# Kernel tuning notes

Measured on AMD Instinct MI355X. Metric: run time of the kernel, lower is better.

## Reference

```python
import jax, jax.numpy as jnp
import numpy as np

I, T, L, E, H, W = 256, 256, 32, 128, 7, 7

def setup_inputs() -> dict:
    key = jax.random.key(0)
    k1, k2, k3 = jax.random.split(key, 3)
    image_features = jax.random.normal(k1, (I, E, H, W), dtype=jnp.float32)
    text_features = jax.random.normal(k2, (T, L, E), dtype=jnp.float32)
    text_length = jax.random.randint(k3, (T,), 1, L + 1, dtype=jnp.int32)
    logit_neg_log_temperature = jnp.asarray(-np.log(0.07), dtype=jnp.float32)
    return {
        "image_features": image_features,
        "text_features": text_features,
        "text_length": text_length,
        "logit_neg_log_temperature": logit_neg_log_temperature,
    }

def reference(image_features, text_features, text_length, logit_neg_log_temperature):
    # image_features: [I, E, H, W]; text_features: [T, L, E]
    i, e, h, w = image_features.shape
    img = image_features.reshape(i, e, h * w)            # [I, E, HW]
    # cross-modal similarity per (image, text, token, patch): [I, T, L, HW]
    sim = jnp.einsum('iep,tle->itlp', img, text_features)
    # max over patches, then sum over tokens, normalized by caption length
    match_max = jnp.max(sim, axis=3)                     # [I, T, L]
    match = jnp.sum(match_max, axis=2) / text_length.astype(match_max.dtype)  # [I, T]
    logit_scale = jnp.exp(logit_neg_log_temperature)
    logits_per_image = match * logit_scale
    logits_per_text = match.T * logit_scale
    return (logits_per_image, logits_per_text)
```

## Files before the change

kernel.cpp:

```cpp
#include <hip/hip_runtime.h>
#include <hip/hip_bf16.h>

typedef __attribute__((ext_vector_type(8)))  short bf16x8;
typedef __attribute__((ext_vector_type(16))) float f32x16;

#define I_N 256
#define T_N 256
#define L_N 32
#define E_N 128
#define P_N 49
#define TG  4

__global__ __launch_bounds__(256) void pack_all(const float* __restrict__ txt,
                                                const float* __restrict__ img,
                                                unsigned short* __restrict__ bpre,
                                                unsigned short* __restrict__ apre) {
    const int bid = blockIdx.x;
    if (bid < 512) {
        int gid  = bid * 256 + threadIdx.x;
        int lane = gid & 63;
        int ks   = (gid >> 6) & 7;
        int t    = gid >> 9;
        int l    = lane & 31;
        int e0   = ks * 16 + (lane >> 5) * 8;
        const float* src = txt + (t * L_N + l) * E_N + e0;
        union { unsigned short u[8]; bf16x8 v; } o;
        #pragma unroll
        for (int j = 0; j < 8; ++j) {
            __hip_bfloat16 h = __float2bfloat16(src[j]);
            o.u[j] = *reinterpret_cast<unsigned short*>(&h);
        }
        ((bf16x8*)bpre)[gid] = o.v;
    } else {
        int gid   = (bid - 512) * 256 + threadIdx.x;
        int lane  = gid & 63;
        int ks    = (gid >> 6) & 7;
        int pt    = (gid >> 9) & 1;
        int i     = gid >> 10;
        int patch = pt * 32 + (lane & 31);
        int e0    = ks * 16 + (lane >> 5) * 8;
        const float* src = img + i * (E_N * P_N) + e0 * P_N + patch;
        union { unsigned short u[8]; bf16x8 v; } o;
        #pragma unroll
        for (int j = 0; j < 8; ++j) {
            float x = (patch < P_N) ? src[j * P_N] : 0.0f;
            __hip_bfloat16 h = __float2bfloat16(x);
            o.u[j] = *reinterpret_cast<unsigned short*>(&h);
        }
        ((bf16x8*)apre)[gid] = o.v;
    }
}

__global__ __launch_bounds__(256) void clip_mfma(
    const unsigned short* __restrict__ apre,
    const unsigned short* __restrict__ bpre,
    const int*   __restrict__ tlen,
    const float* __restrict__ nlt,
    float*       __restrict__ out) {

    __shared__ short sB[2][TG * 8 * 512];

    const int wid  = threadIdx.x >> 6;
    const int lane = threadIdx.x & 63;
    const int i    = blockIdx.y * 4 + wid;
    const int t0   = blockIdx.x * 16;
    const float scale = expf(nlt[0]);
    const bool  lo32  = (lane < 32);

    bf16x8 af[2][8];
    const bf16x8* ap = (const bf16x8*)apre + (size_t)i * 16 * 64;
    #pragma unroll
    for (int pt = 0; pt < 2; ++pt)
        #pragma unroll
        for (int ks = 0; ks < 8; ++ks)
            af[pt][ks] = ap[(pt * 8 + ks) * 64 + lane];

    auto stage = [&](int buf, int g) {
        #pragma unroll
        for (int q = 0; q < 8; ++q) {
            int fl = wid * 8 + q;
            int t  = t0 + g * TG + (fl >> 3);
            int f  = fl & 7;
            const unsigned short* src = bpre + ((size_t)(t * 8 + f)) * 512 + lane * 8;
            short* dst = &sB[buf][fl * 512];
            __builtin_amdgcn_global_load_lds(
                (const __attribute__((address_space(1))) unsigned int*)(const void*)src,
                (__attribute__((address_space(3))) unsigned int*)(void*)dst, 16, 0, 0);
        }
    };

    auto reduceT = [&](f32x16 (&a)[2], int t) {
        float m = a[0][0];
        #pragma unroll
        for (int r = 1; r < 16; ++r) m = fmaxf(m, a[0][r]);
        #pragma unroll
        for (int r = 0; r < 8; ++r)  m = fmaxf(m, a[1][r]);
        m = fmaxf(m, lo32 ? a[1][8] : -INFINITY);
        m = fmaxf(m, __shfl_xor(m, 32));
        float s = m;
        #pragma unroll
        for (int off = 1; off <= 16; off <<= 1)
            s += __shfl_xor(s, off);
        if (lane == 0) {
            float match = (s / (float)tlen[t]) * scale;
            out[i * T_N + t]             = match;
            out[I_N * T_N + t * I_N + i] = match;
        }
    };

    bf16x8 bf[2][8];
    f32x16 acc[2][2];

    stage(0, 0);
    __syncthreads();

    #pragma unroll
    for (int tx = 0; tx < 16; ++tx) {
        const int p   = tx & 1;
        const int gg  = tx >> 2;
        const int txg = tx & 3;

        if ((tx & 3) == 0) {
            if (tx > 0) __syncthreads();
            if (gg + 1 < 4) stage((gg + 1) & 1, gg + 1);
        }

        const bf16x8* bfp = (const bf16x8*)&sB[gg & 1][0];
        #pragma unroll
        for (int ks = 0; ks < 8; ++ks)
            bf[p][ks] = bfp[(txg * 8 + ks) * 64 + lane];

        #pragma unroll
        for (int pt = 0; pt < 2; ++pt)
            #pragma unroll
            for (int r = 0; r < 16; ++r)
                acc[p][pt][r] = 0.0f;

        #pragma unroll
        for (int ks = 0; ks < 8; ++ks)
            #pragma unroll
            for (int pt = 0; pt < 2; ++pt)
                acc[p][pt] = __builtin_amdgcn_mfma_f32_32x32x16_bf16(
                    af[pt][ks], bf[p][ks], acc[p][pt], 0, 0, 0);

        if (tx > 0) reduceT(acc[1 - p], t0 + tx - 1);
    }
    reduceT(acc[1], t0 + 15);
}

extern "C" void kernel_launch(void* const* d_in, const int* in_sizes, int n_in,
                              void* d_out, int out_size, void* d_ws, size_t ws_size,
                              hipStream_t stream) {
    const float* img  = (const float*)d_in[0];
    const float* txt  = (const float*)d_in[1];
    const int*   tlen = (const int*)d_in[2];
    const float* nlt  = (const float*)d_in[3];
    float*       out  = (float*)d_out;

    unsigned short* bpre = (unsigned short*)d_ws;
    unsigned short* apre = (unsigned short*)((char*)d_ws + (2u << 20));

    pack_all<<<1536, 256, 0, stream>>>(txt, img, bpre, apre);

    dim3 grid(16, 64);
    clip_mfma<<<grid, 256, 0, stream>>>(apre, bpre, tlen, nlt, out);
}
```

Before: 45.13 us.

## Software-pipeline LDS B-fragment loads ahead of MFMA and prefetch two stages

Restructures the t-loop so the B fragments for the next text are loaded from LDS while the current MFMA chain runs, using explicit ping-pong register sets instead of array indexing. It stages two text groups up front and issues the next global-to-LDS stage right after each barrier. MFMA sections are wrapped with s_setprio to favour matrix issue across waves. This aims to hide LDS read latency and staging latency behind compute, at the cost of extra register pressure from the doubled B fragments and more complex barrier placement.

```diff
diff --git a/kernel.cpp b/kernel.cpp
--- a/kernel.cpp
+++ b/kernel.cpp
@@ -89,6 +89,29 @@
         }
     };
 
+    auto loadB = [&](bf16x8 (&bf)[8], int buf, int txg) {
+        const bf16x8* bfp = (const bf16x8*)&sB[buf][0];
+        #pragma unroll
+        for (int ks = 0; ks < 8; ++ks)
+            bf[ks] = bfp[(txg * 8 + ks) * 64 + lane];
+    };
+
+    auto mfmaT = [&](f32x16 (&acc)[2], bf16x8 (&bf)[8]) {
+        #pragma unroll
+        for (int pt = 0; pt < 2; ++pt)
+            #pragma unroll
+            for (int r = 0; r < 16; ++r)
+                acc[pt][r] = 0.0f;
+        __builtin_amdgcn_s_setprio(1);
+        #pragma unroll
+        for (int ks = 0; ks < 8; ++ks)
+            #pragma unroll
+            for (int pt = 0; pt < 2; ++pt)
+                acc[pt] = __builtin_amdgcn_mfma_f32_32x32x16_bf16(
+                    af[pt][ks], bf[ks], acc[pt], 0, 0, 0);
+        __builtin_amdgcn_s_setprio(0);
+    };
+
     auto reduceT = [&](f32x16 (&a)[2], int t) {
         float m = a[0][0];
         #pragma unroll
@@ -108,44 +131,34 @@
         }
     };
 
-    bf16x8 bf[2][8];
-    f32x16 acc[2][2];
+    bf16x8 bfA[8], bfB[8];
+    f32x16 accA[2], accB[2];
 
     stage(0, 0);
+    stage(1, 1);
     __syncthreads();
+    loadB(bfA, 0, 0);
+
+    auto slot = [&](int tx, bf16x8 (&bfC)[8], f32x16 (&accC)[2],
+                    bf16x8 (&bfN)[8], f32x16 (&accP)[2]) {
+        const int g   = tx >> 2;
+        const int txg = tx & 3;
+        mfmaT(accC, bfC);
+        if (txg < 3) loadB(bfN, g & 1, txg + 1);
+        if (tx > 0)  reduceT(accP, t0 + tx - 1);
+        if (txg == 3 && tx + 1 < 16) {
+            __syncthreads();
+            if (g + 2 < 4) stage(g & 1, g + 2);
+            loadB(bfN, (g + 1) & 1, 0);
+        }
+    };
 
     #pragma unroll
-    for (int tx = 0; tx < 16; ++tx) {
-        const int p   = tx & 1;
-        const int gg  = tx >> 2;
-        const int txg = tx & 3;
-
-        if ((tx & 3) == 0) {
-            if (tx > 0) __syncthreads();
-            if (gg + 1 < 4) stage((gg + 1) & 1, gg + 1);
-        }
-
-        const bf16x8* bfp = (const bf16x8*)&sB[gg & 1][0];
-        #pragma unroll
-        for (int ks = 0; ks < 8; ++ks)
-            bf[p][ks] = bfp[(txg * 8 + ks) * 64 + lane];
-
-        #pragma unroll
-        for (int pt = 0; pt < 2; ++pt)
-            #pragma unroll
-            for (int r = 0; r < 16; ++r)
-                acc[p][pt][r] = 0.0f;
-
-        #pragma unroll
-        for (int ks = 0; ks < 8; ++ks)
-            #pragma unroll
-            for (int pt = 0; pt < 2; ++pt)
-                acc[p][pt] = __builtin_amdgcn_mfma_f32_32x32x16_bf16(
-                    af[pt][ks], bf[p][ks], acc[p][pt], 0, 0, 0);
-
-        if (tx > 0) reduceT(acc[1 - p], t0 + tx - 1);
+    for (int pr = 0; pr < 8; ++pr) {
+        slot(2 * pr,     bfA, accA, bfB, accB);
+        slot(2 * pr + 1, bfB, accB, bfA, accA);
     }
-    reduceT(acc[1], t0 + 15);
+    reduceT(accB, t0 + 15);
 }
 
 extern "C" void kernel_launch(void* const* d_in, const int* in_sizes, int n_in,
```

After: 47.03 us. 1.04x slower.

## Load text fragments directly from global, drop LDS staging and software pipelining

Applied to the files above, without the earlier changes.

Removes the double-buffered LDS staging via global_load_lds and the barriers between groups. Each wave now loads its B fragments straight from global memory (L2-cached) inside a non-unrolled loop. The kernel gets an occupancy hint of 3 blocks per CU and raises wave priority around the MFMA chain. This removes LDS traffic and block-wide syncs and should lower register pressure, but each wave re-reads B from global/L2 and loses the overlap between loads and the previous tile's reduction.

```diff
diff --git a/kernel.cpp b/kernel.cpp
--- a/kernel.cpp
+++ b/kernel.cpp
@@ -9,7 +9,6 @@
 #define L_N 32
 #define E_N 128
 #define P_N 49
-#define TG  4
 
 __global__ __launch_bounds__(256) void pack_all(const float* __restrict__ txt,
                                                 const float* __restrict__ img,
@@ -51,14 +50,12 @@
     }
 }
 
-__global__ __launch_bounds__(256) void clip_mfma(
+__global__ __launch_bounds__(256, 3) void clip_mfma(
     const unsigned short* __restrict__ apre,
     const unsigned short* __restrict__ bpre,
     const int*   __restrict__ tlen,
     const float* __restrict__ nlt,
     float*       __restrict__ out) {
-
-    __shared__ short sB[2][TG * 8 * 512];
 
     const int wid  = threadIdx.x >> 6;
     const int lane = threadIdx.x & 63;
@@ -75,77 +72,48 @@
         for (int ks = 0; ks < 8; ++ks)
             af[pt][ks] = ap[(pt * 8 + ks) * 64 + lane];
 
-    auto stage = [&](int buf, int g) {
+    const bf16x8* bp = (const bf16x8*)bpre;
+
+    #pragma unroll 1
+    for (int tx = 0; tx < 16; ++tx) {
+        const int t = t0 + tx;
+
+        bf16x8 bf[8];
+        const bf16x8* tb = bp + (size_t)t * 8 * 64;
         #pragma unroll
-        for (int q = 0; q < 8; ++q) {
-            int fl = wid * 8 + q;
-            int t  = t0 + g * TG + (fl >> 3);
-            int f  = fl & 7;
-            const unsigned short* src = bpre + ((size_t)(t * 8 + f)) * 512 + lane * 8;
-            short* dst = &sB[buf][fl * 512];
-            __builtin_amdgcn_global_load_lds(
-                (const __attribute__((address_space(1))) unsigned int*)(const void*)src,
-                (__attribute__((address_space(3))) unsigned int*)(void*)dst, 16, 0, 0);
+        for (int ks = 0; ks < 8; ++ks)
+            bf[ks] = tb[ks * 64 + lane];
+
+        f32x16 a0, a1;
+        #pragma unroll
+        for (int r = 0; r < 16; ++r) { a0[r] = 0.0f; a1[r] = 0.0f; }
+
+        __builtin_amdgcn_s_setprio(1);
+        #pragma unroll
+        for (int ks = 0; ks < 8; ++ks) {
+            a0 = __builtin_amdgcn_mfma_f32_32x32x16_bf16(af[0][ks], bf[ks], a0, 0, 0, 0);
+            a1 = __builtin_amdgcn_mfma_f32_32x32x16_bf16(af[1][ks], bf[ks], a1, 0, 0, 0);
         }
-    };
+        __builtin_amdgcn_s_setprio(0);
 
-    auto reduceT = [&](f32x16 (&a)[2], int t) {
-        float m = a[0][0];
+        float m = a0[0];
         #pragma unroll
-        for (int r = 1; r < 16; ++r) m = fmaxf(m, a[0][r]);
+        for (int r = 1; r < 16; ++r) m = fmaxf(m, a0[r]);
         #pragma unroll
-        for (int r = 0; r < 8; ++r)  m = fmaxf(m, a[1][r]);
-        m = fmaxf(m, lo32 ? a[1][8] : -INFINITY);
+        for (int r = 0; r < 8; ++r)  m = fmaxf(m, a1[r]);
+        m = fmaxf(m, lo32 ? a1[8] : -INFINITY);
         m = fmaxf(m, __shfl_xor(m, 32));
         float s = m;
         #pragma unroll
         for (int off = 1; off <= 16; off <<= 1)
             s += __shfl_xor(s, off);
+
         if (lane == 0) {
             float match = (s / (float)tlen[t]) * scale;
             out[i * T_N + t]             = match;
             out[I_N * T_N + t * I_N + i] = match;
         }
-    };
-
-    bf16x8 bf[2][8];
-    f32x16 acc[2][2];
-
-    stage(0, 0);
-    __syncthreads();
-
-    #pragma unroll
-    for (int tx = 0; tx < 16; ++tx) {
-        const int p   = tx & 1;
-        const int gg  = tx >> 2;
-        const int txg = tx & 3;
-
-        if ((tx & 3) == 0) {
-            if (tx > 0) __syncthreads();
-            if (gg + 1 < 4) stage((gg + 1) & 1, gg + 1);
-        }
-
-        const bf16x8* bfp = (const bf16x8*)&sB[gg & 1][0];
-        #pragma unroll
-        for (int ks = 0; ks < 8; ++ks)
-            bf[p][ks] = bfp[(txg * 8 + ks) * 64 + lane];
-
-        #pragma unroll
-        for (int pt = 0; pt < 2; ++pt)
-            #pragma unroll
-            for (int r = 0; r < 16; ++r)
-                acc[p][pt][r] = 0.0f;
-
-        #pragma unroll
-        for (int ks = 0; ks < 8; ++ks)
-            #pragma unroll
-            for (int pt = 0; pt < 2; ++pt)
-                acc[p][pt] = __builtin_amdgcn_mfma_f32_32x32x16_bf16(
-                    af[pt][ks], bf[p][ks], acc[p][pt], 0, 0, 0);
-
-        if (tx > 0) reduceT(acc[1 - p], t0 + tx - 1);
     }
-    reduceT(acc[1], t0 + 15);
 }
 
 extern "C" void kernel_launch(void* const* d_in, const int* in_sizes, int n_in,
```

Measured after the change: 46.90 us. 3.9% more time.
